# Kernel optimization log

Hardware: AMD Instinct MI355X
Metric: run time of the kernel (lower is better)

The kernel has to match this reference:

```python
import jax, jax.numpy as jnp
import numpy as np

N_NODES = 100000
N_EDGES = 600000
N_GRAPHS = 64
DIM_IN = 128


def setup_inputs() -> dict:
    key = jax.random.key(0)
    ks = jax.random.split(key, 12)
    s = 0.05
    return {
        "feat": jax.random.normal(ks[0], (N_NODES, DIM_IN), jnp.float32),
        "Wself1": jax.random.normal(ks[1], (DIM_IN, 100), jnp.float32) * s,
        "Wneigh1": jax.random.normal(ks[2], (DIM_IN, 100), jnp.float32) * s,
        "b1": jnp.zeros((100,), jnp.float32),
        "Wself2": jax.random.normal(ks[3], (100, 20), jnp.float32) * s,
        "Wneigh2": jax.random.normal(ks[4], (100, 20), jnp.float32) * s,
        "b2": jnp.zeros((20,), jnp.float32),
        "fc1_w": jax.random.normal(ks[5], (20, 10), jnp.float32) * s,
        "fc1_b": jnp.zeros((10,), jnp.float32),
        "fc2_w": jax.random.normal(ks[6], (10, 1), jnp.float32) * s,
        "fc2_b": jnp.zeros((1,), jnp.float32),
        "src": jax.random.randint(ks[7], (N_EDGES,), 0, N_NODES, jnp.int32),
        "dst": jax.random.randint(ks[8], (N_EDGES,), 0, N_NODES, jnp.int32),
        "graph_ids": jnp.sort(jax.random.randint(ks[9], (N_NODES,), 0, N_GRAPHS, jnp.int32)),
    }


def _sage_mean(x, src, dst, inv_deg, Wself, Wneigh, b):
    # DGL SAGEConv(aggr='mean'): fc_self(h) + fc_neigh(mean of in-neighbor feats)
    msg = x[src]  # [E, d] gather
    agg = jax.ops.segment_sum(msg, dst, num_segments=N_NODES) * inv_deg  # [N, d]
    return x @ Wself + agg @ Wneigh + b


def reference(feat, Wself1, Wneigh1, b1, Wself2, Wneigh2, b2,
              fc1_w, fc1_b, fc2_w, fc2_b, src, dst, graph_ids):
    ones_e = jnp.ones((src.shape[0],), feat.dtype)
    deg = jax.ops.segment_sum(ones_e, dst, num_segments=N_NODES)
    inv_deg = (1.0 / jnp.maximum(deg, 1.0))[:, None]  # zero in-degree -> agg stays 0

    h = jax.nn.relu(_sage_mean(feat, src, dst, inv_deg, Wself1, Wneigh1, b1))
    h = jax.nn.relu(_sage_mean(h, src, dst, inv_deg, Wself2, Wneigh2, b2))

    # dgl.mean_nodes: per-graph mean over nodes
    ones_n = jnp.ones((h.shape[0],), h.dtype)
    counts = jax.ops.segment_sum(ones_n, graph_ids, num_segments=N_GRAPHS)
    hg = jax.ops.segment_sum(h, graph_ids, num_segments=N_GRAPHS) / jnp.maximum(counts, 1.0)[:, None]

    out = jax.nn.relu(hg @ fc1_w + fc1_b) @ fc2_w + fc2_b  # [G, 1]
    return out
```

## Files before the change

### kernel.cpp

```cpp
#include <hip/hip_runtime.h>
#include <cstddef>

#define N_NODES  100000
#define N_EDGES  600000
#define N_GRAPHS 64

__device__ __forceinline__ void atomAddF(float* p, float v) {
    unsafeAtomicAdd(p, v);
}

__device__ __forceinline__ float f4get(const float4& v, int i) {
    return i == 0 ? v.x : i == 1 ? v.y : i == 2 ? v.z : v.w;
}

typedef __attribute__((address_space(1))) void GV;
typedef __attribute__((address_space(3))) void LV;
__device__ __forceinline__ void gload16(const float* g, float* l) {
    __builtin_amdgcn_global_load_lds((GV*)g, (LV*)l, 16, 0, 0);
}

__global__ __launch_bounds__(256) void deg_count(const int* __restrict__ dst,
                                                 int* __restrict__ deg) {
    int e = blockIdx.x * 256 + threadIdx.x;
    if (e < N_EDGES) atomicAdd(deg + dst[e], 1);
}

__global__ __launch_bounds__(256)
void alloc_ranges(const int* __restrict__ deg, int* __restrict__ beg,
                  int* __restrict__ cur, int* __restrict__ counter) {
    int n = blockIdx.x * 256 + threadIdx.x;
    int d = (n < N_NODES) ? deg[n] : 0;
    int lane = threadIdx.x & 63, wid = threadIdx.x >> 6;
    int incl = d;
#pragma unroll
    for (int o = 1; o < 64; o <<= 1) {
        int v = __shfl_up(incl, o);
        if (lane >= o) incl += v;
    }
    __shared__ int wsum[4];
    __shared__ int blockBase;
    if (lane == 63) wsum[wid] = incl;
    __syncthreads();
    if (threadIdx.x == 0) {
        int tot = wsum[0] + wsum[1] + wsum[2] + wsum[3];
        blockBase = atomicAdd(counter, tot);
    }
    __syncthreads();
    int base = blockBase;
    for (int w = 0; w < wid; ++w) base += wsum[w];
    int start = base + incl - d;
    if (n < N_NODES) { beg[n] = start; cur[n] = start; }
}

__global__ __launch_bounds__(256)
void csr_fill(const int* __restrict__ src, const int* __restrict__ dst,
              int* __restrict__ cur, int* __restrict__ csr_src) {
    int e = blockIdx.x * 256 + threadIdx.x;
    if (e >= N_EDGES) return;
    int p = atomicAdd(cur + dst[e], 1);
    csr_src[p] = src[e];
}

__global__ __launch_bounds__(256, 6)
void gemm1(const float* __restrict__ feat, const float* __restrict__ Wself,
           const float* __restrict__ Wneigh,
           float* __restrict__ S1, float* __restrict__ N1) {
    __shared__ float As[40 * 16];
    __shared__ float Bs[16][200];
    const int tid  = threadIdx.x;
    const int m0   = blockIdx.x * 40;
    const int wave = tid >> 6;
    const int lane = tid & 63;
    const bool active = tid < 250;
    const int tr  = tid / 25;
    const int tcc = tid % 25;
    const int sw  = tr & 3;

    float4 acc0[4], acc1[4];
#pragma unroll
    for (int i = 0; i < 4; ++i) {
        acc0[i] = make_float4(0.f, 0.f, 0.f, 0.f);
        acc1[i] = make_float4(0.f, 0.f, 0.f, 0.f);
    }

    for (int kt = 0; kt < 8; ++kt) {
        const int k0 = kt * 16;
        if (kt) __syncthreads();

        if (lane < 40) {
            int u  = wave * 40 + lane;
            int r  = u >> 2;
            int k4 = (u & 3) ^ ((r >> 2) & 3);
            gload16(feat + (size_t)(m0 + r) * 128 + k0 + k4 * 4, &As[wave * 160]);
        }
        for (int idx = tid; idx < 800; idx += 256) {
            int k = idx / 50, n4 = idx % 50;
            int n = n4 * 4;
            int gk = k0 + k;
            float4 v;
            if (n < 100) v = *reinterpret_cast<const float4*>(Wself + gk * 100 + n);
            else         v = *reinterpret_cast<const float4*>(Wneigh + gk * 100 + (n - 100));
            *reinterpret_cast<float4*>(&Bs[k][n]) = v;
        }
        __syncthreads();

        if (active) {
            const int abase = tr * 64;
#pragma unroll
            for (int g = 0; g < 4; ++g) {
                const int ac = ((g ^ sw) << 2);
                const float4 a0 = *reinterpret_cast<const float4*>(&As[abase +  0 + ac]);
                const float4 a1 = *reinterpret_cast<const float4*>(&As[abase + 16 + ac]);
                const float4 a2 = *reinterpret_cast<const float4*>(&As[abase + 32 + ac]);
                const float4 a3 = *reinterpret_cast<const float4*>(&As[abase + 48 + ac]);
#pragma unroll
                for (int kl = 0; kl < 4; ++kl) {
                    const int k = g * 4 + kl;
                    const float4 b0 = *reinterpret_cast<const float4*>(&Bs[k][tcc * 4]);
                    const float4 b1 = *reinterpret_cast<const float4*>(&Bs[k][100 + tcc * 4]);
                    const float v0 = f4get(a0, kl), v1 = f4get(a1, kl);
                    const float v2 = f4get(a2, kl), v3 = f4get(a3, kl);
                    acc0[0].x = fmaf(v0, b0.x, acc0[0].x); acc0[0].y = fmaf(v0, b0.y, acc0[0].y);
                    acc0[0].z = fmaf(v0, b0.z, acc0[0].z); acc0[0].w = fmaf(v0, b0.w, acc0[0].w);
                    acc1[0].x = fmaf(v0, b1.x, acc1[0].x); acc1[0].y = fmaf(v0, b1.y, acc1[0].y);
                    acc1[0].z = fmaf(v0, b1.z, acc1[0].z); acc1[0].w = fmaf(v0, b1.w, acc1[0].w);
                    acc0[1].x = fmaf(v1, b0.x, acc0[1].x); acc0[1].y = fmaf(v1, b0.y, acc0[1].y);
                    acc0[1].z = fmaf(v1, b0.z, acc0[1].z); acc0[1].w = fmaf(v1, b0.w, acc0[1].w);
                    acc1[1].x = fmaf(v1, b1.x, acc1[1].x); acc1[1].y = fmaf(v1, b1.y, acc1[1].y);
                    acc1[1].z = fmaf(v1, b1.z, acc1[1].z); acc1[1].w = fmaf(v1, b1.w, acc1[1].w);
                    acc0[2].x = fmaf(v2, b0.x, acc0[2].x); acc0[2].y = fmaf(v2, b0.y, acc0[2].y);
                    acc0[2].z = fmaf(v2, b0.z, acc0[2].z); acc0[2].w = fmaf(v2, b0.w, acc0[2].w);
                    acc1[2].x = fmaf(v2, b1.x, acc1[2].x); acc1[2].y = fmaf(v2, b1.y, acc1[2].y);
                    acc1[2].z = fmaf(v2, b1.z, acc1[2].z); acc1[2].w = fmaf(v2, b1.w, acc1[2].w);
                    acc0[3].x = fmaf(v3, b0.x, acc0[3].x); acc0[3].y = fmaf(v3, b0.y, acc0[3].y);
                    acc0[3].z = fmaf(v3, b0.z, acc0[3].z); acc0[3].w = fmaf(v3, b0.w, acc0[3].w);
                    acc1[3].x = fmaf(v3, b1.x, acc1[3].x); acc1[3].y = fmaf(v3, b1.y, acc1[3].y);
                    acc1[3].z = fmaf(v3, b1.z, acc1[3].z); acc1[3].w = fmaf(v3, b1.w, acc1[3].w);
                }
            }
        }
    }

    if (active) {
        const int c = tcc * 4;
#pragma unroll
        for (int i = 0; i < 4; ++i) {
            int gr = m0 + tr * 4 + i;
            *reinterpret_cast<float4*>(S1 + (size_t)gr * 100 + c) = acc0[i];
            *reinterpret_cast<float4*>(N1 + (size_t)gr * 100 + c) = acc1[i];
        }
    }
}

__global__ __launch_bounds__(256)
void agg1_gemm2(const float* __restrict__ N1, const float* __restrict__ S1,
                const float* __restrict__ b1, const int* __restrict__ csr_src,
                const int* __restrict__ beg, const int* __restrict__ cur,
                const float* __restrict__ Ws2, const float* __restrict__ Wn2,
                float* __restrict__ S2, float* __restrict__ N2) {
    __shared__ float Hs[8][104];
    __shared__ float Bs2[100][40];
    const int tid  = threadIdx.x;
    const int nloc = tid >> 5;
    const int c4   = tid & 31;
    const int n    = blockIdx.x * 8 + nloc;

    for (int idx = tid; idx < 1000; idx += 256) {
        int k = idx / 10;
        int col = (idx % 10) * 4;
        float4 v;
        if (col < 20) v = *reinterpret_cast<const float4*>(Ws2 + k * 20 + col);
        else          v = *reinterpret_cast<const float4*>(Wn2 + k * 20 + (col - 20));
        *reinterpret_cast<float4*>(&Bs2[k][col]) = v;
    }

    if (c4 < 25) {
        int b = beg[n], end = cur[n];
        float4 acc = make_float4(0.f, 0.f, 0.f, 0.f);
        int j = b;
        for (; j + 3 < end; j += 4) {
            int s0 = csr_src[j], s1 = csr_src[j + 1], s2 = csr_src[j + 2], s3 = csr_src[j + 3];
            float4 v0 = *reinterpret_cast<const float4*>(N1 + (size_t)s0 * 100 + c4 * 4);
            float4 v1 = *reinterpret_cast<const float4*>(N1 + (size_t)s1 * 100 + c4 * 4);
            float4 v2 = *reinterpret_cast<const float4*>(N1 + (size_t)s2 * 100 + c4 * 4);
            float4 v3 = *reinterpret_cast<const float4*>(N1 + (size_t)s3 * 100 + c4 * 4);
            acc.x += v0.x + v1.x; acc.y += v0.y + v1.y;
            acc.z += v0.z + v1.z; acc.w += v0.w + v1.w;
            acc.x += v2.x + v3.x; acc.y += v2.y + v3.y;
            acc.z += v2.z + v3.z; acc.w += v2.w + v3.w;
        }
        for (; j + 1 < end; j += 2) {
            int s0 = csr_src[j], s1 = csr_src[j + 1];
            float4 v0 = *reinterpret_cast<const float4*>(N1 + (size_t)s0 * 100 + c4 * 4);
            float4 v1 = *reinterpret_cast<const float4*>(N1 + (size_t)s1 * 100 + c4 * 4);
            acc.x += v0.x + v1.x; acc.y += v0.y + v1.y;
            acc.z += v0.z + v1.z; acc.w += v0.w + v1.w;
        }
        if (j < end) {
            int s = csr_src[j];
            float4 v = *reinterpret_cast<const float4*>(N1 + (size_t)s * 100 + c4 * 4);
            acc.x += v.x; acc.y += v.y; acc.z += v.z; acc.w += v.w;
        }
        float inv = 1.0f / (float)max(end - b, 1);
        float4 s  = *reinterpret_cast<const float4*>(S1 + (size_t)n * 100 + c4 * 4);
        float4 bb = *reinterpret_cast<const float4*>(b1 + c4 * 4);
        float4 h;
        h.x = fmaxf(fmaf(acc.x, inv, s.x) + bb.x, 0.f);
        h.y = fmaxf(fmaf(acc.y, inv, s.y) + bb.y, 0.f);
        h.z = fmaxf(fmaf(acc.z, inv, s.z) + bb.z, 0.f);
        h.w = fmaxf(fmaf(acc.w, inv, s.w) + bb.w, 0.f);
        *reinterpret_cast<float4*>(&Hs[nloc][c4 * 4]) = h;
    }
    __syncthreads();

    for (int idx = tid; idx < 320; idx += 256) {
        int nl = idx / 40, col = idx % 40;
        float a = 0.f;
#pragma unroll 4
        for (int k = 0; k < 100; ++k)
            a = fmaf(Hs[nl][k], Bs2[k][col], a);
        int gn = blockIdx.x * 8 + nl;
        if (col < 20) S2[(size_t)gn * 20 + col] = a;
        else          N2[(size_t)gn * 20 + (col - 20)] = a;
    }
}

__global__ __launch_bounds__(256)
void aggregate2(const float* __restrict__ N2, const float* __restrict__ S2,
                const float* __restrict__ b2, const int* __restrict__ csr_src,
                const int* __restrict__ beg, const int* __restrict__ cur,
                float* __restrict__ h2) {
    int n  = blockIdx.x * 32 + (threadIdx.x >> 3);
    int c4 = threadIdx.x & 7;
    if (n >= N_NODES || c4 >= 5) return;
    int b = beg[n], end = cur[n];
    float4 acc = make_float4(0.f, 0.f, 0.f, 0.f);
    int j = b;
    for (; j + 3 < end; j += 4) {
        int s0 = csr_src[j], s1 = csr_src[j + 1], s2 = csr_src[j + 2], s3 = csr_src[j + 3];
        float4 v0 = *reinterpret_cast<const float4*>(N2 + (size_t)s0 * 20 + c4 * 4);
        float4 v1 = *reinterpret_cast<const float4*>(N2 + (size_t)s1 * 20 + c4 * 4);
        float4 v2 = *reinterpret_cast<const float4*>(N2 + (size_t)s2 * 20 + c4 * 4);
        float4 v3 = *reinterpret_cast<const float4*>(N2 + (size_t)s3 * 20 + c4 * 4);
        acc.x += v0.x + v1.x; acc.y += v0.y + v1.y;
        acc.z += v0.z + v1.z; acc.w += v0.w + v1.w;
        acc.x += v2.x + v3.x; acc.y += v2.y + v3.y;
        acc.z += v2.z + v3.z; acc.w += v2.w + v3.w;
    }
    for (; j + 1 < end; j += 2) {
        int s0 = csr_src[j], s1 = csr_src[j + 1];
        float4 v0 = *reinterpret_cast<const float4*>(N2 + (size_t)s0 * 20 + c4 * 4);
        float4 v1 = *reinterpret_cast<const float4*>(N2 + (size_t)s1 * 20 + c4 * 4);
        acc.x += v0.x + v1.x; acc.y += v0.y + v1.y;
        acc.z += v0.z + v1.z; acc.w += v0.w + v1.w;
    }
    if (j < end) {
        int s = csr_src[j];
        float4 v = *reinterpret_cast<const float4*>(N2 + (size_t)s * 20 + c4 * 4);
        acc.x += v.x; acc.y += v.y; acc.z += v.z; acc.w += v.w;
    }
    float inv = 1.0f / (float)max(end - b, 1);
    float4 s  = *reinterpret_cast<const float4*>(S2 + (size_t)n * 20 + c4 * 4);
    float4 bb = *reinterpret_cast<const float4*>(b2 + c4 * 4);
    float4 h;
    h.x = fmaxf(fmaf(acc.x, inv, s.x) + bb.x, 0.f);
    h.y = fmaxf(fmaf(acc.y, inv, s.y) + bb.y, 0.f);
    h.z = fmaxf(fmaf(acc.z, inv, s.z) + bb.z, 0.f);
    h.w = fmaxf(fmaf(acc.w, inv, s.w) + bb.w, 0.f);
    *reinterpret_cast<float4*>(h2 + (size_t)n * 20 + c4 * 4) = h;
}

__global__ __launch_bounds__(256)
void pool_kernel(const float* __restrict__ h2, const int* __restrict__ gids,
                 float* __restrict__ pool, float* __restrict__ cnt) {
    int n = blockIdx.x * 256 + threadIdx.x;
    float h[20];
    int g = -1;
    if (n < N_NODES) {
        g = gids[n];
#pragma unroll
        for (int q = 0; q < 5; ++q) {
            float4 v = *reinterpret_cast<const float4*>(h2 + (size_t)n * 20 + q * 4);
            h[q * 4 + 0] = v.x; h[q * 4 + 1] = v.y;
            h[q * 4 + 2] = v.z; h[q * 4 + 3] = v.w;
        }
    } else {
#pragma unroll
        for (int c = 0; c < 20; ++c) h[c] = 0.f;
    }
    unsigned long long act = __ballot(n < N_NODES);
    int gfirst = __shfl(g, 0);
    bool uniform = __all(g == gfirst);
    if (uniform) {
        if (gfirst >= 0) {
#pragma unroll
            for (int c = 0; c < 20; ++c)
                for (int off2 = 32; off2 > 0; off2 >>= 1)
                    h[c] += __shfl_down(h[c], off2);
            if ((threadIdx.x & 63) == 0) {
                for (int c = 0; c < 20; ++c) atomAddF(&pool[gfirst * 20 + c], h[c]);
                atomAddF(&cnt[gfirst], (float)__popcll(act));
            }
        }
    } else if (n < N_NODES) {
        for (int c = 0; c < 20; ++c) atomAddF(&pool[g * 20 + c], h[c]);
        atomAddF(&cnt[g], 1.0f);
    }
}

__global__ __launch_bounds__(64)
void head(const float* __restrict__ pool, const float* __restrict__ cnt,
          const float* __restrict__ fc1w, const float* __restrict__ fc1b,
          const float* __restrict__ fc2w, const float* __restrict__ fc2b,
          float* __restrict__ out) {
    int g = threadIdx.x;
    if (g >= N_GRAPHS) return;
    float inv = 1.0f / fmaxf(cnt[g], 1.0f);
    float hg[20];
    for (int c = 0; c < 20; ++c) hg[c] = pool[g * 20 + c] * inv;
    float o = fc2b[0];
    for (int j = 0; j < 10; ++j) {
        float t = fc1b[j];
        for (int c = 0; c < 20; ++c) t = fmaf(hg[c], fc1w[c * 10 + j], t);
        o = fmaf(fmaxf(t, 0.f), fc2w[j], o);
    }
    out[g] = o;
}

extern "C" void kernel_launch(void* const* d_in, const int* in_sizes, int n_in,
                              void* d_out, int out_size, void* d_ws, size_t ws_size,
                              hipStream_t stream) {
    const float* feat   = (const float*)d_in[0];
    const float* Wself1 = (const float*)d_in[1];
    const float* Wneigh1= (const float*)d_in[2];
    const float* b1     = (const float*)d_in[3];
    const float* Wself2 = (const float*)d_in[4];
    const float* Wneigh2= (const float*)d_in[5];
    const float* b2     = (const float*)d_in[6];
    const float* fc1w   = (const float*)d_in[7];
    const float* fc1b   = (const float*)d_in[8];
    const float* fc2w   = (const float*)d_in[9];
    const float* fc2b   = (const float*)d_in[10];
    const int*   src    = (const int*)d_in[11];
    const int*   dst    = (const int*)d_in[12];
    const int*   gids   = (const int*)d_in[13];
    float* ws = (float*)d_ws;

    float* S1 = ws;
    float* N1 = ws + 10000000;
    float* S2 = ws + 20000000;
    float* N2 = ws + 22000000;
    float* h2 = ws;
    int*   deg  = (int*)(ws + 30000000);
    float* pool = ws + 30100000;
    float* cnt  = ws + 30101280;
    int*   ctr  = (int*)(ws + 30101344);
    int*   beg  = (int*)(ws + 30101360);
    int*   cur  = (int*)(ws + 30201360);
    int*   csr  = (int*)(ws + 30301360);

    hipMemsetAsync(deg, 0, (100000 + 1280 + 64 + 16) * sizeof(float), stream);

    deg_count<<<(N_EDGES + 255) / 256, 256, 0, stream>>>(dst, deg);
    alloc_ranges<<<(N_NODES + 255) / 256, 256, 0, stream>>>(deg, beg, cur, ctr);
    csr_fill<<<(N_EDGES + 255) / 256, 256, 0, stream>>>(src, dst, cur, csr);

    gemm1<<<N_NODES / 40, 256, 0, stream>>>(feat, Wself1, Wneigh1, S1, N1);

    agg1_gemm2<<<N_NODES / 8, 256, 0, stream>>>(N1, S1, b1, csr, beg, cur,
                                                Wself2, Wneigh2, S2, N2);

    aggregate2<<<(N_NODES + 31) / 32, 256, 0, stream>>>(N2, S2, b2, csr, beg, cur, h2);

    pool_kernel<<<(N_NODES + 255) / 256, 256, 0, stream>>>(h2, gids, pool, cnt);

    head<<<1, 64, 0, stream>>>(pool, cnt, fc1w, fc1b, fc2w, fc2b, (float*)d_out);
}
```

Before: 288.8 us.

## Fuse degree count into gemm1 and aggregation-2 with pooling, vectorize LDS reads

The edge in-degree atomics move into the gemm1 kernel, so each block also counts one slice of edges and the separate deg_count launch goes away. The second-layer aggregation and the graph mean-pooling become one kernel, which drops the write and re-read of the h2 buffer and one launch. Pooling reduces across the 8 nodes in a wave with shuffles, then issues per-wave atomics. The layer-2 GEMM inner loop now reads Hs as float4, cutting LDS load instructions. The pooling step adds some shuffle and atomic work inside the aggregation kernel.

```diff
diff --git a/kernel.cpp b/kernel.cpp
--- a/kernel.cpp
+++ b/kernel.cpp
@@ -17,12 +17,6 @@
 typedef __attribute__((address_space(3))) void LV;
 __device__ __forceinline__ void gload16(const float* g, float* l) {
     __builtin_amdgcn_global_load_lds((GV*)g, (LV*)l, 16, 0, 0);
-}
-
-__global__ __launch_bounds__(256) void deg_count(const int* __restrict__ dst,
-                                                 int* __restrict__ deg) {
-    int e = blockIdx.x * 256 + threadIdx.x;
-    if (e < N_EDGES) atomicAdd(deg + dst[e], 1);
 }
 
 __global__ __launch_bounds__(256)
@@ -64,7 +58,8 @@
 __global__ __launch_bounds__(256, 6)
 void gemm1(const float* __restrict__ feat, const float* __restrict__ Wself,
            const float* __restrict__ Wneigh,
-           float* __restrict__ S1, float* __restrict__ N1) {
+           float* __restrict__ S1, float* __restrict__ N1,
+           const int* __restrict__ dst, int* __restrict__ deg) {
     __shared__ float As[40 * 16];
     __shared__ float Bs[16][200];
     const int tid  = threadIdx.x;
@@ -75,6 +70,11 @@
     const int tr  = tid / 25;
     const int tcc = tid % 25;
     const int sw  = tr & 3;
+
+    {
+        int e = blockIdx.x * 256 + tid;
+        if (e < N_EDGES) atomicAdd(deg + dst[e], 1);
+    }
 
     float4 acc0[4], acc1[4];
 #pragma unroll
@@ -216,9 +216,14 @@
     for (int idx = tid; idx < 320; idx += 256) {
         int nl = idx / 40, col = idx % 40;
         float a = 0.f;
-#pragma unroll 4
-        for (int k = 0; k < 100; ++k)
-            a = fmaf(Hs[nl][k], Bs2[k][col], a);
+#pragma unroll 5
+        for (int k4 = 0; k4 < 25; ++k4) {
+            const float4 hv = *reinterpret_cast<const float4*>(&Hs[nl][k4 * 4]);
+            a = fmaf(hv.x, Bs2[k4 * 4 + 0][col], a);
+            a = fmaf(hv.y, Bs2[k4 * 4 + 1][col], a);
+            a = fmaf(hv.z, Bs2[k4 * 4 + 2][col], a);
+            a = fmaf(hv.w, Bs2[k4 * 4 + 3][col], a);
+        }
         int gn = blockIdx.x * 8 + nl;
         if (col < 20) S2[(size_t)gn * 20 + col] = a;
         else          N2[(size_t)gn * 20 + (col - 20)] = a;
@@ -226,85 +231,78 @@
 }
 
 __global__ __launch_bounds__(256)
-void aggregate2(const float* __restrict__ N2, const float* __restrict__ S2,
-                const float* __restrict__ b2, const int* __restrict__ csr_src,
-                const int* __restrict__ beg, const int* __restrict__ cur,
-                float* __restrict__ h2) {
-    int n  = blockIdx.x * 32 + (threadIdx.x >> 3);
-    int c4 = threadIdx.x & 7;
-    if (n >= N_NODES || c4 >= 5) return;
-    int b = beg[n], end = cur[n];
-    float4 acc = make_float4(0.f, 0.f, 0.f, 0.f);
-    int j = b;
-    for (; j + 3 < end; j += 4) {
-        int s0 = csr_src[j], s1 = csr_src[j + 1], s2 = csr_src[j + 2], s3 = csr_src[j + 3];
-        float4 v0 = *reinterpret_cast<const float4*>(N2 + (size_t)s0 * 20 + c4 * 4);
-        float4 v1 = *reinterpret_cast<const float4*>(N2 + (size_t)s1 * 20 + c4 * 4);
-        float4 v2 = *reinterpret_cast<const float4*>(N2 + (size_t)s2 * 20 + c4 * 4);
-        float4 v3 = *reinterpret_cast<const float4*>(N2 + (size_t)s3 * 20 + c4 * 4);
-        acc.x += v0.x + v1.x; acc.y += v0.y + v1.y;
-        acc.z += v0.z + v1.z; acc.w += v0.w + v1.w;
-        acc.x += v2.x + v3.x; acc.y += v2.y + v3.y;
-        acc.z += v2.z + v3.z; acc.w += v2.w + v3.w;
-    }
-    for (; j + 1 < end; j += 2) {
-        int s0 = csr_src[j], s1 = csr_src[j + 1];
-        float4 v0 = *reinterpret_cast<const float4*>(N2 + (size_t)s0 * 20 + c4 * 4);
-        float4 v1 = *reinterpret_cast<const float4*>(N2 + (size_t)s1 * 20 + c4 * 4);
-        acc.x += v0.x + v1.x; acc.y += v0.y + v1.y;
-        acc.z += v0.z + v1.z; acc.w += v0.w + v1.w;
-    }
-    if (j < end) {
-        int s = csr_src[j];
-        float4 v = *reinterpret_cast<const float4*>(N2 + (size_t)s * 20 + c4 * 4);
-        acc.x += v.x; acc.y += v.y; acc.z += v.z; acc.w += v.w;
-    }
-    float inv = 1.0f / (float)max(end - b, 1);
-    float4 s  = *reinterpret_cast<const float4*>(S2 + (size_t)n * 20 + c4 * 4);
-    float4 bb = *reinterpret_cast<const float4*>(b2 + c4 * 4);
-    float4 h;
-    h.x = fmaxf(fmaf(acc.x, inv, s.x) + bb.x, 0.f);
-    h.y = fmaxf(fmaf(acc.y, inv, s.y) + bb.y, 0.f);
-    h.z = fmaxf(fmaf(acc.z, inv, s.z) + bb.z, 0.f);
-    h.w = fmaxf(fmaf(acc.w, inv, s.w) + bb.w, 0.f);
-    *reinterpret_cast<float4*>(h2 + (size_t)n * 20 + c4 * 4) = h;
-}
-
-__global__ __launch_bounds__(256)
-void pool_kernel(const float* __restrict__ h2, const int* __restrict__ gids,
-                 float* __restrict__ pool, float* __restrict__ cnt) {
-    int n = blockIdx.x * 256 + threadIdx.x;
-    float h[20];
-    int g = -1;
-    if (n < N_NODES) {
-        g = gids[n];
-#pragma unroll
-        for (int q = 0; q < 5; ++q) {
-            float4 v = *reinterpret_cast<const float4*>(h2 + (size_t)n * 20 + q * 4);
-            h[q * 4 + 0] = v.x; h[q * 4 + 1] = v.y;
-            h[q * 4 + 2] = v.z; h[q * 4 + 3] = v.w;
-        }
-    } else {
-#pragma unroll
-        for (int c = 0; c < 20; ++c) h[c] = 0.f;
-    }
-    unsigned long long act = __ballot(n < N_NODES);
-    int gfirst = __shfl(g, 0);
+void agg2_pool(const float* __restrict__ N2, const float* __restrict__ S2,
+               const float* __restrict__ b2, const int* __restrict__ csr_src,
+               const int* __restrict__ beg, const int* __restrict__ cur,
+               const int* __restrict__ gids,
+               float* __restrict__ pool, float* __restrict__ cnt) {
+    const int tid  = threadIdx.x;
+    const int n    = blockIdx.x * 32 + (tid >> 3);
+    const int c4   = tid & 7;
+    const bool live = (c4 < 5);
+
+    float4 h = make_float4(0.f, 0.f, 0.f, 0.f);
+    if (live) {
+        int b = beg[n], end = cur[n];
+        float4 acc = make_float4(0.f, 0.f, 0.f, 0.f);
+        int j = b;
+        for (; j + 3 < end; j += 4) {
+            int s0 = csr_src[j], s1 = csr_src[j + 1], s2 = csr_src[j + 2], s3 = csr_src[j + 3];
+            float4 v0 = *reinterpret_cast<const float4*>(N2 + (size_t)s0 * 20 + c4 * 4);
+            float4 v1 = *reinterpret_cast<const float4*>(N2 + (size_t)s1 * 20 + c4 * 4);
+            float4 v2 = *reinterpret_cast<const float4*>(N2 + (size_t)s2 * 20 + c4 * 4);
+            float4 v3 = *reinterpret_cast<const float4*>(N2 + (size_t)s3 * 20 + c4 * 4);
+            acc.x += v0.x + v1.x; acc.y += v0.y + v1.y;
+            acc.z += v0.z + v1.z; acc.w += v0.w + v1.w;
+            acc.x += v2.x + v3.x; acc.y += v2.y + v3.y;
+            acc.z += v2.z + v3.z; acc.w += v2.w + v3.w;
+        }
+        for (; j + 1 < end; j += 2) {
+            int s0 = csr_src[j], s1 = csr_src[j + 1];
+            float4 v0 = *reinterpret_cast<const float4*>(N2 + (size_t)s0 * 20 + c4 * 4);
+            float4 v1 = *reinterpret_cast<const float4*>(N2 + (size_t)s1 * 20 + c4 * 4);
+            acc.x += v0.x + v1.x; acc.y += v0.y + v1.y;
+            acc.z += v0.z + v1.z; acc.w += v0.w + v1.w;
+        }
+        if (j < end) {
+            int s = csr_src[j];
+            float4 v = *reinterpret_cast<const float4*>(N2 + (size_t)s * 20 + c4 * 4);
+            acc.x += v.x; acc.y += v.y; acc.z += v.z; acc.w += v.w;
+        }
+        float inv = 1.0f / (float)max(end - b, 1);
+        float4 s  = *reinterpret_cast<const float4*>(S2 + (size_t)n * 20 + c4 * 4);
+        float4 bb = *reinterpret_cast<const float4*>(b2 + c4 * 4);
+        h.x = fmaxf(fmaf(acc.x, inv, s.x) + bb.x, 0.f);
+        h.y = fmaxf(fmaf(acc.y, inv, s.y) + bb.y, 0.f);
+        h.z = fmaxf(fmaf(acc.z, inv, s.z) + bb.z, 0.f);
+        h.w = fmaxf(fmaf(acc.w, inv, s.w) + bb.w, 0.f);
+    }
+
+    int g = gids[n];
+    int gfirst = __shfl(g, (threadIdx.x & 192));
+    gfirst = __shfl(g, 0);
     bool uniform = __all(g == gfirst);
     if (uniform) {
-        if (gfirst >= 0) {
-#pragma unroll
-            for (int c = 0; c < 20; ++c)
-                for (int off2 = 32; off2 > 0; off2 >>= 1)
-                    h[c] += __shfl_down(h[c], off2);
-            if ((threadIdx.x & 63) == 0) {
-                for (int c = 0; c < 20; ++c) atomAddF(&pool[gfirst * 20 + c], h[c]);
-                atomAddF(&cnt[gfirst], (float)__popcll(act));
-            }
-        }
-    } else if (n < N_NODES) {
-        for (int c = 0; c < 20; ++c) atomAddF(&pool[g * 20 + c], h[c]);
-        atomAddF(&cnt[g], 1.0f);
+#pragma unroll
+        for (int off = 32; off >= 8; off >>= 1) {
+            h.x += __shfl_down(h.x, off);
+            h.y += __shfl_down(h.y, off);
+            h.z += __shfl_down(h.z, off);
+            h.w += __shfl_down(h.w, off);
+        }
+        if ((tid & 63) < 5) {
+            atomAddF(&pool[gfirst * 20 + c4 * 4 + 0], h.x);
+            atomAddF(&pool[gfirst * 20 + c4 * 4 + 1], h.y);
+            atomAddF(&pool[gfirst * 20 + c4 * 4 + 2], h.z);
+            atomAddF(&pool[gfirst * 20 + c4 * 4 + 3], h.w);
+        }
+        if ((tid & 63) == 0) atomAddF(&cnt[gfirst], 8.0f);
+    } else if (live) {
+        atomAddF(&pool[g * 20 + c4 * 4 + 0], h.x);
+        atomAddF(&pool[g * 20 + c4 * 4 + 1], h.y);
+        atomAddF(&pool[g * 20 + c4 * 4 + 2], h.z);
+        atomAddF(&pool[g * 20 + c4 * 4 + 3], h.w);
+        if (c4 == 0) atomAddF(&cnt[g], 1.0f);
     }
 }
 
@@ -350,7 +348,6 @@
     float* N1 = ws + 10000000;
     float* S2 = ws + 20000000;
     float* N2 = ws + 22000000;
-    float* h2 = ws;
     int*   deg  = (int*)(ws + 30000000);
     float* pool = ws + 30100000;
     float* cnt  = ws + 30101280;
@@ -361,18 +358,16 @@
 
     hipMemsetAsync(deg, 0, (100000 + 1280 + 64 + 16) * sizeof(float), stream);
 
-    deg_count<<<(N_EDGES + 255) / 256, 256, 0, stream>>>(dst, deg);
+    gemm1<<<N_NODES / 40, 256, 0, stream>>>(feat, Wself1, Wneigh1, S1, N1, dst, deg);
+
     alloc_ranges<<<(N_NODES + 255) / 256, 256, 0, stream>>>(deg, beg, cur, ctr);
     csr_fill<<<(N_EDGES + 255) / 256, 256, 0, stream>>>(src, dst, cur, csr);
 
-    gemm1<<<N_NODES / 40, 256, 0, stream>>>(feat, Wself1, Wneigh1, S1, N1);
-
     agg1_gemm2<<<N_NODES / 8, 256, 0, stream>>>(N1, S1, b1, csr, beg, cur,
                                                 Wself2, Wneigh2, S2, N2);
 
-    aggregate2<<<(N_NODES + 31) / 32, 256, 0, stream>>>(N2, S2, b2, csr, beg, cur, h2);
-
-    pool_kernel<<<(N_NODES + 255) / 256, 256, 0, stream>>>(h2, gids, pool, cnt);
+    agg2_pool<<<N_NODES / 32, 256, 0, stream>>>(N2, S2, b2, csr, beg, cur,
+                                                gids, pool, cnt);
 
     head<<<1, 64, 0, stream>>>(pool, cnt, fc1w, fc1b, fc2w, fc2b, (float*)d_out);
 }
```

New measurement: 307.1 us. 1.06x slower.
